# Optimization experiments

Hardware: AMD Instinct MI355X
Metric: run time of the kernel (lower is better)

Reference implementation:

```python
import jax, jax.numpy as jnp
import numpy as np
import math

N_HEADS = 16
FACTOR = 5

def setup_inputs() -> dict:
    key = jax.random.key(0)
    ks = jax.random.split(key, 9)
    B, T, D = 4, 2048, 1024
    w = lambda k: jax.random.normal(k, (D, D), dtype=jnp.float32) * 0.02
    return {
        "x": jax.random.normal(ks[0], (B, T, D), dtype=jnp.float32),
        "Wq": w(ks[1]), "bq": jnp.zeros((D,), jnp.float32),
        "Wk": w(ks[2]), "bk": jnp.zeros((D,), jnp.float32),
        "Wv": w(ks[3]), "bv": jnp.zeros((D,), jnp.float32),
        "Wo": w(ks[4]), "bo": jnp.zeros((D,), jnp.float32),
    }

def reference(x, Wq, bq, Wk, bk, Wv, bv, Wo, bo):
    B, T, D = x.shape
    H = N_HEADS
    hd = D // H
    scale = hd ** (-0.5)

    def proj(W, b):
        # [B,T,D] -> [B,H,T,hd]
        return (x @ W + b).reshape(B, T, H, hd).transpose(0, 2, 1, 3)

    q = proj(Wq, bq)
    k = proj(Wk, bk)
    v = proj(Wv, bv)

    # top-u query selection by L1 norm per (b,h)
    u = min(int(FACTOR * math.log(T)), T)
    q_norm = jnp.sum(jnp.abs(q), axis=-1)          # [B,H,T]
    _, idx = jax.lax.top_k(q_norm, u)              # [B,H,u]

    # gather selected queries; compute only the u selected score rows
    q_sel = jnp.take_along_axis(q, idx[..., None], axis=2)  # [B,H,u,hd]
    sel_scores = jnp.einsum('bhud,bhtd->bhut', q_sel, k) * scale  # [B,H,u,T]

    # causal mask for selected rows: key pos j attends iff j <= query pos
    causal = jnp.arange(T)[None, None, None, :] <= idx[..., None]  # [B,H,u,T]
    sel_scores = jnp.where(causal, sel_scores, -jnp.inf)

    attn = jax.nn.softmax(sel_scores, axis=-1)     # dropout omitted (eval)
    sel_out = jnp.einsum('bhut,bhtd->bhud', attn, v)  # [B,H,u,hd]

    # scatter selected rows back into zeros (non-selected rows stay 0)
    bi = jnp.arange(B)[:, None, None]
    hi = jnp.arange(H)[None, :, None]
    attn_out = jnp.zeros((B, H, T, hd), x.dtype).at[bi, hi, idx].set(sel_out)

    out = attn_out.transpose(0, 2, 1, 3).reshape(B, T, D)
    return out @ Wo + bo
```

## Files before the change

kernel.cpp:

```cpp
#include <hip/hip_runtime.h>
#include <hip/hip_bf16.h>
#include <math.h>

#define B_  4
#define T_  2048
#define D_  1024
#define H_  16
#define HD_ 64
#define U_  38
#define M_  (B_*T_)
#define NCW_ 32
#define NC_ 144

typedef __attribute__((ext_vector_type(8))) short bf16x8;
typedef __attribute__((ext_vector_type(4))) float f32x4;

__device__ __forceinline__ short f2b(float f) {
    __hip_bfloat16 b = __float2bfloat16(f);
    return *(short*)&b;
}
__device__ __forceinline__ float b2f(short s) {
    __hip_bfloat16 b = *(__hip_bfloat16*)&s;
    return __bfloat162float(b);
}
__device__ __forceinline__ unsigned pack2(float lo, float hi) {
    unsigned a = (unsigned short)f2b(lo);
    unsigned b = ((unsigned)(unsigned short)f2b(hi)) << 16;
    return a | b;
}

__device__ __forceinline__ void gload16(const void* g, void* l) {
    __builtin_amdgcn_global_load_lds(
        (const __attribute__((address_space(1))) unsigned int*)g,
        (__attribute__((address_space(3))) unsigned int*)l,
        16, 0, 0);
}

__global__ __launch_bounds__(256) void convx_kernel(
    const float* __restrict__ x, short* __restrict__ xh, short* __restrict__ xl)
{
    const size_t i = ((size_t)blockIdx.x * 256 + threadIdx.x) * 4;
    float4 v = *(const float4*)(x + i);
    short4 h, l;
    h.x = f2b(v.x); l.x = f2b(v.x - b2f(h.x));
    h.y = f2b(v.y); l.y = f2b(v.y - b2f(h.y));
    h.z = f2b(v.z); l.z = f2b(v.z - b2f(h.z));
    h.w = f2b(v.w); l.w = f2b(v.w - b2f(h.w));
    *(short4*)(xh + i) = h;
    *(short4*)(xl + i) = l;
}

__global__ __launch_bounds__(256) void convw_kernel(
    const float* __restrict__ Wq, const float* __restrict__ Wk,
    const float* __restrict__ Wv, const float* __restrict__ Wo,
    short* __restrict__ wq2, short* __restrict__ wkvt, short* __restrict__ wot)
{
    __shared__ float tile[32][33];
    const int which = blockIdx.z;
    const float* W = which == 0 ? Wq : (which == 1 ? Wk : (which == 2 ? Wv : Wo));
    const int k0 = blockIdx.y * 32, n0 = blockIdx.x * 32;
    const int tx = threadIdx.x & 31, ty = threadIdx.x >> 5;
    #pragma unroll
    for (int r = ty; r < 32; r += 8)
        tile[r][tx] = W[(size_t)(k0 + r) * D_ + n0 + tx];
    __syncthreads();
    #pragma unroll
    for (int r = ty; r < 32; r += 8) {
        float v = tile[tx][r];
        size_t o = (size_t)(n0 + r) * D_ + k0 + tx;
        if (which == 0) {
            short h = f2b(v);
            wq2[o] = h;
            wq2[o + 1048576] = f2b(v - b2f(h));
        } else if (which == 3) {
            wot[o] = f2b(v);
        } else {
            wkvt[(size_t)(which - 1) * D_ * D_ + o] = f2b(v);
        }
    }
}

__global__ __launch_bounds__(256) void gemm_fused(
    const short* __restrict__ xh, const short* __restrict__ wq2,
    const short* __restrict__ wkvt,
    const float* __restrict__ bq, const float* __restrict__ bk,
    const float* __restrict__ bv,
    float* __restrict__ qnorm, short* __restrict__ kb, short* __restrict__ vt)
{
    __shared__ short As[128 * 64];
    __shared__ short Bs[128 * 64];
    const int bid = blockIdx.x;
    const bool isQ = bid < 512;
    const int tid = threadIdx.x, wid = tid >> 6, lane = tid & 63;
    const int l15 = lane & 15, gr = lane >> 4;
    const int lb = isQ ? bid : bid - 512;
    const int m0 = (lb & 63) * 128;
    const int n0 = (lb >> 6) * 128;
    const bool isK = !isQ && (n0 < D_);
    const int wr = (wid >> 1) * 64, wc = (wid & 1) * 64;

    f32x4 acc[4][4];
    #pragma unroll
    for (int i = 0; i < 4; ++i)
        #pragma unroll
        for (int j = 0; j < 4; ++j)
            acc[i][j] = (f32x4){0.f, 0.f, 0.f, 0.f};

    const short* Asrc = xh;
    const short* Bsrc = isQ ? wq2 : wkvt;

    for (int kt = 0; kt < 16; ++kt) {
        const int ka = kt * 64;
        #pragma unroll
        for (int i = 0; i < 4; ++i) {
            const int e = tid + i * 256;
            const int row = e >> 3;
            const int soff = ((e & 7) ^ (row & 7)) * 8;
            gload16(Asrc + (size_t)(m0 + row) * D_ + ka + soff,
                    (char*)As + i * 4096 + wid * 1024);
            gload16(Bsrc + (size_t)(n0 + row) * D_ + ka + soff,
                    (char*)Bs + i * 4096 + wid * 1024);
        }
        __syncthreads();
        #pragma unroll
        for (int ks = 0; ks < 2; ++ks) {
            bf16x8 a[4], b[4];
            #pragma unroll
            for (int i = 0; i < 4; ++i)
                a[i] = *(bf16x8*)((char*)As + (wr + i * 16 + l15) * 128
                                   + (((ks << 2) | gr) ^ (l15 & 7)) * 16);
            #pragma unroll
            for (int j = 0; j < 4; ++j)
                b[j] = *(bf16x8*)((char*)Bs + (wc + j * 16 + l15) * 128
                                   + (((ks << 2) | gr) ^ (l15 & 7)) * 16);
            if (isK) {
                #pragma unroll
                for (int i = 0; i < 4; ++i)
                    #pragma unroll
                    for (int j = 0; j < 4; ++j)
                        acc[i][j] = __builtin_amdgcn_mfma_f32_16x16x32_bf16(b[j], a[i], acc[i][j], 0, 0, 0);
            } else {
                #pragma unroll
                for (int i = 0; i < 4; ++i)
                    #pragma unroll
                    for (int j = 0; j < 4; ++j)
                        acc[i][j] = __builtin_amdgcn_mfma_f32_16x16x32_bf16(a[i], b[j], acc[i][j], 0, 0, 0);
            }
        }
        __syncthreads();
    }

    if (isQ) {
        const int h = (n0 + wc) >> 6;
        #pragma unroll
        for (int i = 0; i < 4; ++i)
            #pragma unroll
            for (int r = 0; r < 4; ++r) {
                int row = m0 + wr + i * 16 + gr * 4 + r;
                float s = 0.f;
                #pragma unroll
                for (int j = 0; j < 4; ++j) {
                    int col = n0 + wc + j * 16 + l15;
                    s += fabsf(acc[i][j][r] + bq[col]);
                }
                s += __shfl_xor(s, 1);
                s += __shfl_xor(s, 2);
                s += __shfl_xor(s, 4);
                s += __shfl_xor(s, 8);
                if (l15 == 0) {
                    int b = row >> 11, t = row & (T_ - 1);
                    qnorm[((size_t)b * H_ + h) * T_ + t] = s;
                }
            }
    } else if (isK) {
        #pragma unroll
        for (int i = 0; i < 4; ++i)
            #pragma unroll
            for (int j = 0; j < 4; ++j) {
                const int m = m0 + wr + i * 16 + l15;
                const int bb = m >> 11, t = m & (T_ - 1);
                const int n = n0 + wc + j * 16 + gr * 4;
                const int hh = n >> 6, dd = n & 63;
                float4 bias = *(const float4*)(bk + n);
                short4 pk;
                pk.x = f2b(acc[i][j][0] + bias.x);
                pk.y = f2b(acc[i][j][1] + bias.y);
                pk.z = f2b(acc[i][j][2] + bias.z);
                pk.w = f2b(acc[i][j][3] + bias.w);
                *(short4*)(kb + (((size_t)bb * H_ + hh) * T_ + t) * HD_ + dd) = pk;
            }
    } else {
        #pragma unroll
        for (int i = 0; i < 4; ++i)
            #pragma unroll
            for (int j = 0; j < 4; ++j) {
                const int col = n0 + wc + j * 16 + l15;
                const int rowb = m0 + wr + i * 16 + gr * 4;
                const int bb = rowb >> 11, t0 = rowb & (T_ - 1);
                const int cc2 = col - D_;
                const int hh = cc2 >> 6, dd = cc2 & 63;
                const float bias = bv[cc2];
                short4 pk;
                pk.x = f2b(acc[i][j][0] + bias);
                pk.y = f2b(acc[i][j][1] + bias);
                pk.z = f2b(acc[i][j][2] + bias);
                pk.w = f2b(acc[i][j][3] + bias);
                *(short4*)(vt + (((size_t)bb * H_ + hh) * HD_ + dd) * T_ + t0) = pk;
            }
    }
}

__global__ __launch_bounds__(64) void cand_kernel(
    const float* __restrict__ qnorm, int* __restrict__ cand)
{
    const int g = blockIdx.x;
    const int lane = threadIdx.x;
    unsigned v[32];
    const float* src = qnorm + (size_t)g * T_ + lane * 32;
    #pragma unroll
    for (int i = 0; i < 32; i += 4) {
        float4 t = *(const float4*)(src + i);
        v[i] = __float_as_uint(t.x); v[i + 1] = __float_as_uint(t.y);
        v[i + 2] = __float_as_uint(t.z); v[i + 3] = __float_as_uint(t.w);
    }
    unsigned lo = 0, hi = 0x7F800000u;
    while (lo < hi) {
        unsigned mid = lo + ((hi - lo) >> 1);
        int c = 0;
        #pragma unroll
        for (int i = 0; i < 32; ++i) c += (v[i] >= mid) ? 1 : 0;
        #pragma unroll
        for (int off = 1; off < 64; off <<= 1) c += __shfl_xor(c, off);
        if (c <= NC_) hi = mid; else lo = mid + 1;
    }
    const unsigned tau = lo;
    int myc = 0;
    #pragma unroll
    for (int i = 0; i < 32; ++i) myc += (v[i] >= tau) ? 1 : 0;
    int inc = myc;
    for (int off = 1; off < 64; off <<= 1) {
        int n = __shfl_up(inc, off);
        if (lane >= off) inc += n;
    }
    const int total = __shfl(inc, 63);
    int pos = inc - myc;
    #pragma unroll
    for (int i = 0; i < 32; ++i)
        if (v[i] >= tau) cand[g * NC_ + pos++] = lane * 32 + i;
    for (int p = total + lane; p < NC_; p += 64)
        cand[g * NC_ + p] = -1;
}

__global__ __launch_bounds__(64) void recheck_kernel(
    const short* __restrict__ xh, const short* __restrict__ xl,
    const short* __restrict__ wq2, const float* __restrict__ bq,
    const int* __restrict__ cand,
    float* __restrict__ cnorm, short* __restrict__ candq)
{
    const int blk = blockIdx.x;
    const int g = blk / 9, rt = blk % 9;
    const int b = g >> 4, h = g & 15;
    const int lane = threadIdx.x, l15 = lane & 15, gr = lane >> 4;

    const int aslot = rt * 16 + l15;
    int at = cand[g * NC_ + aslot];
    const size_t arow = ((size_t)b * T_ + (at < 0 ? 0 : at)) * D_;

    f32x4 acc[4];
    #pragma unroll
    for (int j = 0; j < 4; ++j) acc[j] = (f32x4){0.f, 0.f, 0.f, 0.f};

    const short* wqh = wq2;
    const short* wql = wq2 + 1048576;
    for (int kt = 0; kt < 32; ++kt) {
        const int k0 = kt * 32 + gr * 8;
        bf16x8 ah = *(const bf16x8*)(xh + arow + k0);
        bf16x8 al = *(const bf16x8*)(xl + arow + k0);
        #pragma unroll
        for (int j = 0; j < 4; ++j) {
            const size_t wrow = (size_t)(h * HD_ + j * 16 + l15) * D_ + k0;
            bf16x8 bh = *(const bf16x8*)(wqh + wrow);
            bf16x8 bl = *(const bf16x8*)(wql + wrow);
            acc[j] = __builtin_amdgcn_mfma_f32_16x16x32_bf16(ah, bh, acc[j], 0, 0, 0);
            acc[j] = __builtin_amdgcn_mfma_f32_16x16x32_bf16(ah, bl, acc[j], 0, 0, 0);
            acc[j] = __builtin_amdgcn_mfma_f32_16x16x32_bf16(al, bh, acc[j], 0, 0, 0);
        }
    }

    #pragma unroll
    for (int r = 0; r < 4; ++r) {
        const int slot = rt * 16 + gr * 4 + r;
        float s = 0.f;
        #pragma unroll
        for (int j = 0; j < 4; ++j) {
            const int col = j * 16 + l15;
            float val = acc[j][r] + bq[h * HD_ + col];
            candq[((size_t)g * NC_ + slot) * HD_ + col] = f2b(val);
            s += fabsf(val);
        }
        s += __shfl_xor(s, 1);
        s += __shfl_xor(s, 2);
        s += __shfl_xor(s, 4);
        s += __shfl_xor(s, 8);
        if (l15 == 0) {
            int ct = cand[g * NC_ + slot];
            cnorm[g * NC_ + slot] = (ct < 0) ? -3e38f : s;
        }
    }
}

__global__ __launch_bounds__(64) void topk38_kernel(
    const float* __restrict__ cnorm, const int* __restrict__ cand,
    int* __restrict__ idxb, int* __restrict__ slotb)
{
    const int g = blockIdx.x;
    const int lane = threadIdx.x;
    float v[3]; int tt[3];
    #pragma unroll
    for (int i = 0; i < 3; ++i) {
        int s = lane + 64 * i;
        if (s < NC_) {
            v[i] = cnorm[g * NC_ + s];
            int c = cand[g * NC_ + s];
            tt[i] = (c < 0) ? (1 << 30) : c;
            if (c < 0) v[i] = -3e38f;
        } else { v[i] = -3e38f; tt[i] = 1 << 30; }
    }
    for (int it = 0; it < U_; ++it) {
        float bv = -3e38f; int bt = 1 << 30, bi = 0;
        #pragma unroll
        for (int i = 0; i < 3; ++i) {
            bool better = (v[i] > bv) || (v[i] == bv && tt[i] < bt);
            if (better) { bv = v[i]; bt = tt[i]; bi = i; }
        }
        int bs = lane + 64 * bi;
        for (int off = 32; off; off >>= 1) {
            float ov = __shfl_xor(bv, off);
            int ot = __shfl_xor(bt, off);
            int os = __shfl_xor(bs, off);
            if (ov > bv || (ov == bv && ot < bt)) { bv = ov; bt = ot; bs = os; }
        }
        if (lane == 0) { idxb[g * U_ + it] = bt; slotb[g * 40 + it] = bs; }
        if ((bs & 63) == lane) {
            int wi = bs >> 6;
            if (wi == 0) v[0] = -3e38f;
            else if (wi == 1) v[1] = -3e38f;
            else v[2] = -3e38f;
        }
    }
}

__global__ __launch_bounds__(256) void attn_part(
    const short* __restrict__ candq, const int* __restrict__ slotb,
    const short* __restrict__ kb, const short* __restrict__ vt,
    const int* __restrict__ idxb,
    float* __restrict__ pm, float* __restrict__ pl, float* __restrict__ po)
{
    __shared__ short qs[48 * 72];
    __shared__ short pls[4][48 * 72];
    __shared__ int   sidx[48];
    const int bid = blockIdx.x;
    const int g = bid & 63;
    const int c = bid >> 6;
    const int tid = threadIdx.x, wid = tid >> 6, lane = tid & 63;
    const int l15 = lane & 15, gr = lane >> 4;
    const int cw = c * 4 + wid;
    const int j0w = cw * 64;

    if (tid < 48) sidx[tid] = (tid < U_) ? idxb[g * U_ + tid] : 0;
    __syncthreads();
    for (int e = tid; e < 48 * 16; e += 256) {
        int u = e >> 4, d4 = e & 15;
        short4 v = make_short4(0, 0, 0, 0);
        if (u < U_) {
            int slot = slotb[g * 40 + u];
            v = *(const short4*)(candq + ((size_t)g * NC_ + slot) * HD_ + d4 * 4);
        }
        *(short4*)&qs[u * 72 + d4 * 4] = v;
    }
    __syncthreads();

    int su[3];
    #pragma unroll
    for (int uf = 0; uf < 3; ++uf) su[uf] = sidx[uf * 16 + l15];

    f32x4 accs[3][4];
    #pragma unroll
    for (int uf = 0; uf < 3; ++uf)
        #pragma unroll
        for (int jf = 0; jf < 4; ++jf)
            accs[uf][jf] = (f32x4){0.f, 0.f, 0.f, 0.f};

    bf16x8 ka[4][2], qb[3][2];
    #pragma unroll
    for (int jf = 0; jf < 4; ++jf)
        #pragma unroll
        for (int ks = 0; ks < 2; ++ks)
            ka[jf][ks] = *(const bf16x8*)(kb + ((size_t)g * T_ + j0w + jf * 16 + l15) * HD_ + ks * 32 + gr * 8);
    #pragma unroll
    for (int uf = 0; uf < 3; ++uf)
        #pragma unroll
        for (int ks = 0; ks < 2; ++ks)
            qb[uf][ks] = *(bf16x8*)&qs[(uf * 16 + l15) * 72 + ks * 32 + gr * 8];

    #pragma unroll
    for (int uf = 0; uf < 3; ++uf)
        #pragma unroll
        for (int jf = 0; jf < 4; ++jf) {
            accs[uf][jf] = __builtin_amdgcn_mfma_f32_16x16x32_bf16(ka[jf][0], qb[uf][0], accs[uf][jf], 0, 0, 0);
            accs[uf][jf] = __builtin_amdgcn_mfma_f32_16x16x32_bf16(ka[jf][1], qb[uf][1], accs[uf][jf], 0, 0, 0);
        }

    #pragma unroll
    for (int uf = 0; uf < 3; ++uf) {
        float mm = -3e38f;
        #pragma unroll
        for (int jf = 0; jf < 4; ++jf)
            #pragma unroll
            for (int r = 0; r < 4; ++r) {
                int j = j0w + jf * 16 + gr * 4 + r;
                float s = accs[uf][jf][r] * 0.125f;
                s = (j <= su[uf]) ? s : -1e30f;
                accs[uf][jf][r] = s;
                mm = fmaxf(mm, s);
            }
        mm = fmaxf(mm, __shfl_xor(mm, 16));
        mm = fmaxf(mm, __shfl_xor(mm, 32));
        float ll = 0.f;
        #pragma unroll
        for (int jf = 0; jf < 4; ++jf)
            #pragma unroll
            for (int r = 0; r < 4; ++r) {
                float e = __expf(accs[uf][jf][r] - mm);
                accs[uf][jf][r] = e;
                ll += e;
            }
        ll += __shfl_xor(ll, 16);
        ll += __shfl_xor(ll, 32);
        if (gr == 0) {
            int u = uf * 16 + l15;
            if (u < U_) {
                pm[((size_t)g * NCW_ + cw) * U_ + u] = mm;
                pl[((size_t)g * NCW_ + cw) * U_ + u] = ll;
            }
        }
    }

    short* pw = &pls[wid][0];
    #pragma unroll
    for (int uf = 0; uf < 3; ++uf)
        #pragma unroll
        for (int jf = 0; jf < 4; ++jf) {
            uint2 wv;
            wv.x = pack2(accs[uf][jf][0], accs[uf][jf][1]);
            wv.y = pack2(accs[uf][jf][2], accs[uf][jf][3]);
            *(uint2*)&pw[(uf * 16 + l15) * 72 + jf * 16 + gr * 4] = wv;
        }

    bf16x8 va[4][2], pb[3][2];
    #pragma unroll
    for (int df = 0; df < 4; ++df)
        #pragma unroll
        for (int ks = 0; ks < 2; ++ks)
            va[df][ks] = *(const bf16x8*)(vt + ((size_t)g * HD_ + df * 16 + l15) * T_ + j0w + ks * 32 + gr * 8);
    #pragma unroll
    for (int uf = 0; uf < 3; ++uf)
        #pragma unroll
        for (int ks = 0; ks < 2; ++ks)
            pb[uf][ks] = *(bf16x8*)&pw[(uf * 16 + l15) * 72 + ks * 32 + gr * 8];

    f32x4 acco[4][3];
    #pragma unroll
    for (int df = 0; df < 4; ++df)
        #pragma unroll
        for (int uf = 0; uf < 3; ++uf)
            acco[df][uf] = (f32x4){0.f, 0.f, 0.f, 0.f};
    #pragma unroll
    for (int df = 0; df < 4; ++df)
        #pragma unroll
        for (int uf = 0; uf < 3; ++uf) {
            acco[df][uf] = __builtin_amdgcn_mfma_f32_16x16x32_bf16(va[df][0], pb[uf][0], acco[df][uf], 0, 0, 0);
            acco[df][uf] = __builtin_amdgcn_mfma_f32_16x16x32_bf16(va[df][1], pb[uf][1], acco[df][uf], 0, 0, 0);
        }

    #pragma unroll
    for (int df = 0; df < 4; ++df)
        #pragma unroll
        for (int uf = 0; uf < 3; ++uf) {
            int u = uf * 16 + l15;
            if (u < U_) {
                float4 o;
                o.x = acco[df][uf][0]; o.y = acco[df][uf][1];
                o.z = acco[df][uf][2]; o.w = acco[df][uf][3];
                *(float4*)(po + (((size_t)g * NCW_ + cw) * U_ + u) * HD_ + df * 16 + gr * 4) = o;
            }
        }
}

__global__ __launch_bounds__(256) void attn_combine(
    const float* __restrict__ pm, const float* __restrict__ pl,
    const float* __restrict__ po, float* __restrict__ selo)
{
    const int g = blockIdx.x;
    const int u = blockIdx.y * 4 + (threadIdx.x >> 6);
    const int d = threadIdx.x & 63;
    if (u >= U_) return;

    const float* pmg = pm + (size_t)g * NCW_ * U_ + u;
    const float* plg = pl + (size_t)g * NCW_ * U_ + u;

    float mc[NCW_];
    #pragma unroll
    for (int c = 0; c < NCW_; ++c) mc[c] = pmg[(size_t)c * U_];
    float m = -3e38f;
    #pragma unroll
    for (int c = 0; c < NCW_; ++c) m = fmaxf(m, mc[c]);

    float w[NCW_];
    #pragma unroll
    for (int c = 0; c < NCW_; ++c) w[c] = __expf(mc[c] - m);

    float l = 0.f;
    #pragma unroll
    for (int c = 0; c < NCW_; ++c) l += plg[(size_t)c * U_] * w[c];

    float o = 0.f;
    #pragma unroll
    for (int c = 0; c < NCW_; ++c)
        o += po[(((size_t)g * NCW_ + c) * U_ + u) * HD_ + d] * w[c];

    selo[((size_t)g * U_ + u) * HD_ + d] = o / l;
}

__global__ __launch_bounds__(256) void fill_kernel(
    const float* __restrict__ bo, float* __restrict__ out)
{
    const size_t i = (size_t)blockIdx.x * 256 + threadIdx.x;
    float4 bv = *(const float4*)(bo + ((i & 255) << 2));
    *(float4*)(out + i * 4) = bv;
}

__global__ __launch_bounds__(256) void oproj_kernel(
    const float* __restrict__ selo, const int* __restrict__ idxb,
    const short* __restrict__ wot, float* __restrict__ out)
{
    __shared__ short sel[48 * 72];
    __shared__ int st[48];
    const int g = blockIdx.x;
    const int b = g >> 4, h = g & 15;
    const int tid = threadIdx.x, w = tid >> 6, lane = tid & 63;
    const int l15 = lane & 15, gr = lane >> 4;

    for (int e = tid; e < 48 * 16; e += 256) {
        int u = e >> 4, d4 = e & 15;
        short4 v4 = make_short4(0, 0, 0, 0);
        if (u < U_) {
            float4 f = *(const float4*)(selo + ((size_t)g * U_ + u) * HD_ + d4 * 4);
            v4.x = f2b(f.x); v4.y = f2b(f.y); v4.z = f2b(f.z); v4.w = f2b(f.w);
        }
        *(short4*)&sel[u * 72 + d4 * 4] = v4;
    }
    if (tid < 48) st[tid] = (tid < U_) ? idxb[g * U_ + tid] : 0;
    __syncthreads();

    bf16x8 a[3][2];
    #pragma unroll
    for (int uf = 0; uf < 3; ++uf)
        #pragma unroll
        for (int ks = 0; ks < 2; ++ks)
            a[uf][ks] = *(bf16x8*)&sel[(uf * 16 + l15) * 72 + ks * 32 + gr * 8];

    for (int nf = 0; nf < 16; ++nf) {
        const int n0 = w * 256 + nf * 16;
        bf16x8 bf[2];
        #pragma unroll
        for (int ks = 0; ks < 2; ++ks)
            bf[ks] = *(const bf16x8*)(wot + (size_t)(n0 + l15) * D_ + h * HD_ + ks * 32 + gr * 8);
        f32x4 acc[3];
        #pragma unroll
        for (int uf = 0; uf < 3; ++uf) {
            acc[uf] = (f32x4){0.f, 0.f, 0.f, 0.f};
            acc[uf] = __builtin_amdgcn_mfma_f32_16x16x32_bf16(a[uf][0], bf[0], acc[uf], 0, 0, 0);
            acc[uf] = __builtin_amdgcn_mfma_f32_16x16x32_bf16(a[uf][1], bf[1], acc[uf], 0, 0, 0);
        }
        #pragma unroll
        for (int uf = 0; uf < 3; ++uf)
            #pragma unroll
            for (int r = 0; r < 4; ++r) {
                int u = uf * 16 + gr * 4 + r;
                if (u < U_)
                    atomicAdd(out + ((size_t)b * T_ + st[u]) * D_ + n0 + l15, acc[uf][r]);
            }
    }
}

extern "C" void kernel_launch(void* const* d_in, const int* in_sizes, int n_in,
                              void* d_out, int out_size, void* d_ws, size_t ws_size,
                              hipStream_t stream)
{
    const float* x  = (const float*)d_in[0];
    const float* Wq = (const float*)d_in[1];
    const float* bq = (const float*)d_in[2];
    const float* Wk = (const float*)d_in[3];
    const float* bk = (const float*)d_in[4];
    const float* Wv = (const float*)d_in[5];
    const float* bv = (const float*)d_in[6];
    const float* Wo = (const float*)d_in[7];
    const float* bo = (const float*)d_in[8];
    float* out = (float*)d_out;

    char* ws = (char*)d_ws;
    short* xh    = (short*)(ws);
    short* xl    = (short*)(ws + 16777216);
    short* wq2   = (short*)(ws + 33554432);
    short* wkvt  = (short*)(ws + 37748736);
    short* kb    = (short*)(ws + 41943040);
    short* vt    = (short*)(ws + 58720256);
    float* qnorm = (float*)(ws + 75497472);
    int*   idxb  = (int*)  (ws + 76021760);
    float* selo  = (float*)(ws + 76038144);
    int*   cand  = (int*)  (ws + 76660736);
    float* cnorm = (float*)(ws + 76697600);
    int*   slotb = (int*)  (ws + 76734464);
    short* candq = (short*)(ws + 76750848);
    short* wot   = (short*)(ws + 77930496);
    float* po    = (float*)(ws);
    float* pm    = (float*)(ws + 19922944);
    float* pl    = (float*)(ws + 20234240);

    convx_kernel<<<M_ * D_ / 1024, 256, 0, stream>>>(x, xh, xl);
    convw_kernel<<<dim3(32, 32, 4), 256, 0, stream>>>(Wq, Wk, Wv, Wo, wq2, wkvt, wot);
    gemm_fused<<<1536, 256, 0, stream>>>(xh, wq2, wkvt, bq, bk, bv, qnorm, kb, vt);
    cand_kernel<<<B_ * H_, 64, 0, stream>>>(qnorm, cand);
    recheck_kernel<<<B_ * H_ * 9, 64, 0, stream>>>(xh, xl, wq2, bq, cand, cnorm, candq);
    topk38_kernel<<<B_ * H_, 64, 0, stream>>>(cnorm, cand, idxb, slotb);
    attn_part<<<64 * 8, 256, 0, stream>>>(candq, slotb, kb, vt, idxb, pm, pl, po);
    attn_combine<<<dim3(B_ * H_, (U_ + 3) / 4), 256, 0, stream>>>(pm, pl, po, selo);
    fill_kernel<<<(M_ * D_ / 4) / 256, 256, 0, stream>>>(bo, out);
    oproj_kernel<<<B_ * H_, 256, 0, stream>>>(selo, idxb, wot, out);
}
```

Before: 202.7 us.

## Fuse conversion kernels, merge top-k selection stages, reduce attention partials in-block

Merges the x and weight conversion kernels into one launch. Folds candidate selection, the candidate recheck GEMM and the top-38 pick into a single 256-thread block per (batch, head), with intermediates kept in shared memory. Inside attn_part, the four waves' softmax partials are combined in shared memory so only 8 partials per head, not 32, go to global memory for attn_combine. This cuts launch overhead and partial traffic, but the select stage now runs on only 64 blocks, with the 9 recheck tiles spread over 4 waves, which lowers parallelism.

```diff
diff --git a/kernel.cpp b/kernel.cpp
--- a/kernel.cpp
+++ b/kernel.cpp
@@ -9,7 +9,7 @@
 #define HD_ 64
 #define U_  38
 #define M_  (B_*T_)
-#define NCW_ 32
+#define NCB_ 8
 #define NC_ 144
 
 typedef __attribute__((ext_vector_type(8))) short bf16x8;
@@ -36,29 +36,32 @@
         16, 0, 0);
 }
 
-__global__ __launch_bounds__(256) void convx_kernel(
-    const float* __restrict__ x, short* __restrict__ xh, short* __restrict__ xl)
-{
-    const size_t i = ((size_t)blockIdx.x * 256 + threadIdx.x) * 4;
-    float4 v = *(const float4*)(x + i);
-    short4 h, l;
-    h.x = f2b(v.x); l.x = f2b(v.x - b2f(h.x));
-    h.y = f2b(v.y); l.y = f2b(v.y - b2f(h.y));
-    h.z = f2b(v.z); l.z = f2b(v.z - b2f(h.z));
-    h.w = f2b(v.w); l.w = f2b(v.w - b2f(h.w));
-    *(short4*)(xh + i) = h;
-    *(short4*)(xl + i) = l;
-}
-
-__global__ __launch_bounds__(256) void convw_kernel(
+__global__ __launch_bounds__(256) void conv_fused(
+    const float* __restrict__ x,
     const float* __restrict__ Wq, const float* __restrict__ Wk,
     const float* __restrict__ Wv, const float* __restrict__ Wo,
+    short* __restrict__ xh, short* __restrict__ xl,
     short* __restrict__ wq2, short* __restrict__ wkvt, short* __restrict__ wot)
 {
     __shared__ float tile[32][33];
-    const int which = blockIdx.z;
+    const int bid = blockIdx.x;
+    if (bid < 8192) {
+        const size_t i = ((size_t)bid * 256 + threadIdx.x) * 4;
+        float4 v = *(const float4*)(x + i);
+        short4 h, l;
+        h.x = f2b(v.x); l.x = f2b(v.x - b2f(h.x));
+        h.y = f2b(v.y); l.y = f2b(v.y - b2f(h.y));
+        h.z = f2b(v.z); l.z = f2b(v.z - b2f(h.z));
+        h.w = f2b(v.w); l.w = f2b(v.w - b2f(h.w));
+        *(short4*)(xh + i) = h;
+        *(short4*)(xl + i) = l;
+        return;
+    }
+    const int q = bid - 8192;
+    const int which = q >> 10;
+    const int by = (q & 1023) >> 5, bx = q & 31;
     const float* W = which == 0 ? Wq : (which == 1 ? Wk : (which == 2 ? Wv : Wo));
-    const int k0 = blockIdx.y * 32, n0 = blockIdx.x * 32;
+    const int k0 = by * 32, n0 = bx * 32;
     const int tx = threadIdx.x & 31, ty = threadIdx.x >> 5;
     #pragma unroll
     for (int r = ty; r < 32; r += 8)
@@ -210,142 +213,133 @@
     }
 }
 
-__global__ __launch_bounds__(64) void cand_kernel(
-    const float* __restrict__ qnorm, int* __restrict__ cand)
-{
-    const int g = blockIdx.x;
-    const int lane = threadIdx.x;
-    unsigned v[32];
-    const float* src = qnorm + (size_t)g * T_ + lane * 32;
-    #pragma unroll
-    for (int i = 0; i < 32; i += 4) {
-        float4 t = *(const float4*)(src + i);
-        v[i] = __float_as_uint(t.x); v[i + 1] = __float_as_uint(t.y);
-        v[i + 2] = __float_as_uint(t.z); v[i + 3] = __float_as_uint(t.w);
-    }
-    unsigned lo = 0, hi = 0x7F800000u;
-    while (lo < hi) {
-        unsigned mid = lo + ((hi - lo) >> 1);
-        int c = 0;
-        #pragma unroll
-        for (int i = 0; i < 32; ++i) c += (v[i] >= mid) ? 1 : 0;
-        #pragma unroll
-        for (int off = 1; off < 64; off <<= 1) c += __shfl_xor(c, off);
-        if (c <= NC_) hi = mid; else lo = mid + 1;
-    }
-    const unsigned tau = lo;
-    int myc = 0;
-    #pragma unroll
-    for (int i = 0; i < 32; ++i) myc += (v[i] >= tau) ? 1 : 0;
-    int inc = myc;
-    for (int off = 1; off < 64; off <<= 1) {
-        int n = __shfl_up(inc, off);
-        if (lane >= off) inc += n;
-    }
-    const int total = __shfl(inc, 63);
-    int pos = inc - myc;
-    #pragma unroll
-    for (int i = 0; i < 32; ++i)
-        if (v[i] >= tau) cand[g * NC_ + pos++] = lane * 32 + i;
-    for (int p = total + lane; p < NC_; p += 64)
-        cand[g * NC_ + p] = -1;
-}
-
-__global__ __launch_bounds__(64) void recheck_kernel(
+__global__ __launch_bounds__(256) void select_kernel(
+    const float* __restrict__ qnorm,
     const short* __restrict__ xh, const short* __restrict__ xl,
     const short* __restrict__ wq2, const float* __restrict__ bq,
-    const int* __restrict__ cand,
-    float* __restrict__ cnorm, short* __restrict__ candq)
-{
-    const int blk = blockIdx.x;
-    const int g = blk / 9, rt = blk % 9;
+    int* __restrict__ idxb, int* __restrict__ slotb, short* __restrict__ candq)
+{
+    __shared__ int   scand[NC_];
+    __shared__ float scnorm[NC_];
+    const int g = blockIdx.x;
     const int b = g >> 4, h = g & 15;
-    const int lane = threadIdx.x, l15 = lane & 15, gr = lane >> 4;
-
-    const int aslot = rt * 16 + l15;
-    int at = cand[g * NC_ + aslot];
-    const size_t arow = ((size_t)b * T_ + (at < 0 ? 0 : at)) * D_;
-
-    f32x4 acc[4];
-    #pragma unroll
-    for (int j = 0; j < 4; ++j) acc[j] = (f32x4){0.f, 0.f, 0.f, 0.f};
+    const int tid = threadIdx.x, wid = tid >> 6, lane = tid & 63;
+    const int l15 = lane & 15, gr = lane >> 4;
+
+    if (wid == 0) {
+        unsigned v[32];
+        const float* src = qnorm + (size_t)g * T_ + lane * 32;
+        #pragma unroll
+        for (int i = 0; i < 32; i += 4) {
+            float4 t = *(const float4*)(src + i);
+            v[i] = __float_as_uint(t.x); v[i + 1] = __float_as_uint(t.y);
+            v[i + 2] = __float_as_uint(t.z); v[i + 3] = __float_as_uint(t.w);
+        }
+        unsigned lo = 0, hi = 0x7F800000u;
+        while (lo < hi) {
+            unsigned mid = lo + ((hi - lo) >> 1);
+            int c = 0;
+            #pragma unroll
+            for (int i = 0; i < 32; ++i) c += (v[i] >= mid) ? 1 : 0;
+            #pragma unroll
+            for (int off = 1; off < 64; off <<= 1) c += __shfl_xor(c, off);
+            if (c <= NC_) hi = mid; else lo = mid + 1;
+        }
+        const unsigned tau = lo;
+        int myc = 0;
+        #pragma unroll
+        for (int i = 0; i < 32; ++i) myc += (v[i] >= tau) ? 1 : 0;
+        int inc = myc;
+        for (int off = 1; off < 64; off <<= 1) {
+            int n = __shfl_up(inc, off);
+            if (lane >= off) inc += n;
+        }
+        const int total = __shfl(inc, 63);
+        int pos = inc - myc;
+        #pragma unroll
+        for (int i = 0; i < 32; ++i)
+            if (v[i] >= tau) scand[pos++] = lane * 32 + i;
+        for (int p = total + lane; p < NC_; p += 64)
+            scand[p] = -1;
+    }
+    __syncthreads();
 
     const short* wqh = wq2;
     const short* wql = wq2 + 1048576;
-    for (int kt = 0; kt < 32; ++kt) {
-        const int k0 = kt * 32 + gr * 8;
-        bf16x8 ah = *(const bf16x8*)(xh + arow + k0);
-        bf16x8 al = *(const bf16x8*)(xl + arow + k0);
-        #pragma unroll
-        for (int j = 0; j < 4; ++j) {
-            const size_t wrow = (size_t)(h * HD_ + j * 16 + l15) * D_ + k0;
-            bf16x8 bh = *(const bf16x8*)(wqh + wrow);
-            bf16x8 bl = *(const bf16x8*)(wql + wrow);
-            acc[j] = __builtin_amdgcn_mfma_f32_16x16x32_bf16(ah, bh, acc[j], 0, 0, 0);
-            acc[j] = __builtin_amdgcn_mfma_f32_16x16x32_bf16(ah, bl, acc[j], 0, 0, 0);
-            acc[j] = __builtin_amdgcn_mfma_f32_16x16x32_bf16(al, bh, acc[j], 0, 0, 0);
-        }
-    }
-
-    #pragma unroll
-    for (int r = 0; r < 4; ++r) {
-        const int slot = rt * 16 + gr * 4 + r;
-        float s = 0.f;
-        #pragma unroll
-        for (int j = 0; j < 4; ++j) {
-            const int col = j * 16 + l15;
-            float val = acc[j][r] + bq[h * HD_ + col];
-            candq[((size_t)g * NC_ + slot) * HD_ + col] = f2b(val);
-            s += fabsf(val);
-        }
-        s += __shfl_xor(s, 1);
-        s += __shfl_xor(s, 2);
-        s += __shfl_xor(s, 4);
-        s += __shfl_xor(s, 8);
-        if (l15 == 0) {
-            int ct = cand[g * NC_ + slot];
-            cnorm[g * NC_ + slot] = (ct < 0) ? -3e38f : s;
-        }
-    }
-}
-
-__global__ __launch_bounds__(64) void topk38_kernel(
-    const float* __restrict__ cnorm, const int* __restrict__ cand,
-    int* __restrict__ idxb, int* __restrict__ slotb)
-{
-    const int g = blockIdx.x;
-    const int lane = threadIdx.x;
-    float v[3]; int tt[3];
-    #pragma unroll
-    for (int i = 0; i < 3; ++i) {
-        int s = lane + 64 * i;
-        if (s < NC_) {
-            v[i] = cnorm[g * NC_ + s];
-            int c = cand[g * NC_ + s];
-            tt[i] = (c < 0) ? (1 << 30) : c;
-            if (c < 0) v[i] = -3e38f;
-        } else { v[i] = -3e38f; tt[i] = 1 << 30; }
-    }
-    for (int it = 0; it < U_; ++it) {
-        float bv = -3e38f; int bt = 1 << 30, bi = 0;
+    for (int rt = wid; rt < 9; rt += 4) {
+        int at = scand[rt * 16 + l15];
+        const size_t arow = ((size_t)b * T_ + (at < 0 ? 0 : at)) * D_;
+        f32x4 acc[4];
+        #pragma unroll
+        for (int j = 0; j < 4; ++j) acc[j] = (f32x4){0.f, 0.f, 0.f, 0.f};
+        for (int kt = 0; kt < 32; ++kt) {
+            const int k0 = kt * 32 + gr * 8;
+            bf16x8 ah = *(const bf16x8*)(xh + arow + k0);
+            bf16x8 al = *(const bf16x8*)(xl + arow + k0);
+            #pragma unroll
+            for (int j = 0; j < 4; ++j) {
+                const size_t wrow = (size_t)(h * HD_ + j * 16 + l15) * D_ + k0;
+                bf16x8 bh = *(const bf16x8*)(wqh + wrow);
+                bf16x8 bl = *(const bf16x8*)(wql + wrow);
+                acc[j] = __builtin_amdgcn_mfma_f32_16x16x32_bf16(ah, bh, acc[j], 0, 0, 0);
+                acc[j] = __builtin_amdgcn_mfma_f32_16x16x32_bf16(ah, bl, acc[j], 0, 0, 0);
+                acc[j] = __builtin_amdgcn_mfma_f32_16x16x32_bf16(al, bh, acc[j], 0, 0, 0);
+            }
+        }
+        #pragma unroll
+        for (int r = 0; r < 4; ++r) {
+            const int slot = rt * 16 + gr * 4 + r;
+            float s = 0.f;
+            #pragma unroll
+            for (int j = 0; j < 4; ++j) {
+                const int col = j * 16 + l15;
+                float val = acc[j][r] + bq[h * HD_ + col];
+                candq[((size_t)g * NC_ + slot) * HD_ + col] = f2b(val);
+                s += fabsf(val);
+            }
+            s += __shfl_xor(s, 1);
+            s += __shfl_xor(s, 2);
+            s += __shfl_xor(s, 4);
+            s += __shfl_xor(s, 8);
+            if (l15 == 0)
+                scnorm[slot] = (scand[slot] < 0) ? -3e38f : s;
+        }
+    }
+    __syncthreads();
+
+    if (wid == 0) {
+        float v[3]; int tt[3];
         #pragma unroll
         for (int i = 0; i < 3; ++i) {
-            bool better = (v[i] > bv) || (v[i] == bv && tt[i] < bt);
-            if (better) { bv = v[i]; bt = tt[i]; bi = i; }
-        }
-        int bs = lane + 64 * bi;
-        for (int off = 32; off; off >>= 1) {
-            float ov = __shfl_xor(bv, off);
-            int ot = __shfl_xor(bt, off);
-            int os = __shfl_xor(bs, off);
-            if (ov > bv || (ov == bv && ot < bt)) { bv = ov; bt = ot; bs = os; }
-        }
-        if (lane == 0) { idxb[g * U_ + it] = bt; slotb[g * 40 + it] = bs; }
-        if ((bs & 63) == lane) {
-            int wi = bs >> 6;
-            if (wi == 0) v[0] = -3e38f;
-            else if (wi == 1) v[1] = -3e38f;
-            else v[2] = -3e38f;
+            int s = lane + 64 * i;
+            if (s < NC_) {
+                v[i] = scnorm[s];
+                int c = scand[s];
+                tt[i] = (c < 0) ? (1 << 30) : c;
+                if (c < 0) v[i] = -3e38f;
+            } else { v[i] = -3e38f; tt[i] = 1 << 30; }
+        }
+        for (int it = 0; it < U_; ++it) {
+            float bv = -3e38f; int bt = 1 << 30, bi = 0;
+            #pragma unroll
+            for (int i = 0; i < 3; ++i) {
+                bool better = (v[i] > bv) || (v[i] == bv && tt[i] < bt);
+                if (better) { bv = v[i]; bt = tt[i]; bi = i; }
+            }
+            int bs = lane + 64 * bi;
+            for (int off = 32; off; off >>= 1) {
+                float ov = __shfl_xor(bv, off);
+                int ot = __shfl_xor(bt, off);
+                int os = __shfl_xor(bs, off);
+                if (ov > bv || (ov == bv && ot < bt)) { bv = ov; bt = ot; bs = os; }
+            }
+            if (lane == 0) { idxb[g * U_ + it] = bt; slotb[g * 40 + it] = bs; }
+            if ((bs & 63) == lane) {
+                int wi = bs >> 6;
+                if (wi == 0) v[0] = -3e38f;
+                else if (wi == 1) v[1] = -3e38f;
+                else v[2] = -3e38f;
+            }
         }
     }
 }
@@ -357,15 +351,19 @@
     float* __restrict__ pm, float* __restrict__ pl, float* __restrict__ po)
 {
     __shared__ short qs[48 * 72];
-    __shared__ short pls[4][48 * 72];
-    __shared__ int   sidx[48];
+    __shared__ __align__(16) char shbuf[40448];
+    __shared__ int sidx[48];
+    short* pls  = (short*)shbuf;
+    float* redo = (float*)shbuf;
+    float* redm = (float*)(shbuf + 38912);
+    float* redl = (float*)(shbuf + 39680);
+
     const int bid = blockIdx.x;
     const int g = bid & 63;
     const int c = bid >> 6;
     const int tid = threadIdx.x, wid = tid >> 6, lane = tid & 63;
     const int l15 = lane & 15, gr = lane >> 4;
-    const int cw = c * 4 + wid;
-    const int j0w = cw * 64;
+    const int j0w = (c * 4 + wid) * 64;
 
     if (tid < 48) sidx[tid] = (tid < U_) ? idxb[g * U_ + tid] : 0;
     __syncthreads();
@@ -439,14 +437,12 @@
         ll += __shfl_xor(ll, 32);
         if (gr == 0) {
             int u = uf * 16 + l15;
-            if (u < U_) {
-                pm[((size_t)g * NCW_ + cw) * U_ + u] = mm;
-                pl[((size_t)g * NCW_ + cw) * U_ + u] = ll;
-            }
-        }
-    }
-
-    short* pw = &pls[wid][0];
+            redm[wid * 48 + u] = mm;
+            redl[wid * 48 + u] = ll;
+        }
+    }
+
+    short* pw = pls + wid * 48 * 72;
     #pragma unroll
     for (int uf = 0; uf < 3; ++uf)
         #pragma unroll
@@ -482,6 +478,8 @@
             acco[df][uf] = __builtin_amdgcn_mfma_f32_16x16x32_bf16(va[df][0], pb[uf][0], acco[df][uf], 0, 0, 0);
             acco[df][uf] = __builtin_amdgcn_mfma_f32_16x16x32_bf16(va[df][1], pb[uf][1], acco[df][uf], 0, 0, 0);
         }
+
+    __syncthreads();
 
     #pragma unroll
     for (int df = 0; df < 4; ++df)
@@ -492,9 +490,27 @@
                 float4 o;
                 o.x = acco[df][uf][0]; o.y = acco[df][uf][1];
                 o.z = acco[df][uf][2]; o.w = acco[df][uf][3];
-                *(float4*)(po + (((size_t)g * NCW_ + cw) * U_ + u) * HD_ + df * 16 + gr * 4) = o;
-            }
-        }
+                *(float4*)&redo[((size_t)(wid * 38 + u)) * 64 + df * 16 + gr * 4] = o;
+            }
+        }
+    __syncthreads();
+
+    for (int e = tid; e < U_ * 64; e += 256) {
+        int u = e >> 6, d = e & 63;
+        float m0 = redm[u], m1 = redm[48 + u], m2 = redm[96 + u], m3 = redm[144 + u];
+        float m = fmaxf(fmaxf(m0, m1), fmaxf(m2, m3));
+        float e0 = __expf(m0 - m), e1 = __expf(m1 - m), e2 = __expf(m2 - m), e3 = __expf(m3 - m);
+        float l = redl[u] * e0 + redl[48 + u] * e1 + redl[96 + u] * e2 + redl[144 + u] * e3;
+        float o = redo[(size_t)u * 64 + d] * e0
+                + redo[(size_t)(38 + u) * 64 + d] * e1
+                + redo[(size_t)(76 + u) * 64 + d] * e2
+                + redo[(size_t)(114 + u) * 64 + d] * e3;
+        po[((size_t)(g * NCB_ + c) * U_ + u) * HD_ + d] = o;
+        if (d == 0) {
+            pm[(size_t)(g * NCB_ + c) * U_ + u] = m;
+            pl[(size_t)(g * NCB_ + c) * U_ + u] = l;
+        }
+    }
 }
 
 __global__ __launch_bounds__(256) void attn_combine(
@@ -506,28 +522,28 @@
     const int d = threadIdx.x & 63;
     if (u >= U_) return;
 
-    const float* pmg = pm + (size_t)g * NCW_ * U_ + u;
-    const float* plg = pl + (size_t)g * NCW_ * U_ + u;
-
-    float mc[NCW_];
-    #pragma unroll
-    for (int c = 0; c < NCW_; ++c) mc[c] = pmg[(size_t)c * U_];
+    const float* pmg = pm + (size_t)g * NCB_ * U_ + u;
+    const float* plg = pl + (size_t)g * NCB_ * U_ + u;
+
+    float mc[NCB_];
+    #pragma unroll
+    for (int c = 0; c < NCB_; ++c) mc[c] = pmg[(size_t)c * U_];
     float m = -3e38f;
     #pragma unroll
-    for (int c = 0; c < NCW_; ++c) m = fmaxf(m, mc[c]);
-
-    float w[NCW_];
-    #pragma unroll
-    for (int c = 0; c < NCW_; ++c) w[c] = __expf(mc[c] - m);
+    for (int c = 0; c < NCB_; ++c) m = fmaxf(m, mc[c]);
+
+    float w[NCB_];
+    #pragma unroll
+    for (int c = 0; c < NCB_; ++c) w[c] = __expf(mc[c] - m);
 
     float l = 0.f;
     #pragma unroll
-    for (int c = 0; c < NCW_; ++c) l += plg[(size_t)c * U_] * w[c];
+    for (int c = 0; c < NCB_; ++c) l += plg[(size_t)c * U_] * w[c];
 
     float o = 0.f;
     #pragma unroll
-    for (int c = 0; c < NCW_; ++c)
-        o += po[(((size_t)g * NCW_ + c) * U_ + u) * HD_ + d] * w[c];
+    for (int c = 0; c < NCB_; ++c)
+        o += po[(((size_t)g * NCB_ + c) * U_ + u) * HD_ + d] * w[c];
 
     selo[((size_t)g * U_ + u) * HD_ + d] = o / l;
 }
@@ -619,8 +635,6 @@
     float* qnorm = (float*)(ws + 75497472);
     int*   idxb  = (int*)  (ws + 76021760);
     float* selo  = (float*)(ws + 76038144);
-    int*   cand  = (int*)  (ws + 76660736);
-    float* cnorm = (float*)(ws + 76697600);
     int*   slotb = (int*)  (ws + 76734464);
     short* candq = (short*)(ws + 76750848);
     short* wot   = (short*)(ws + 77930496);
@@ -628,13 +642,12 @@
     float* pm    = (float*)(ws + 19922944);
     float* pl    = (float*)(ws + 20234240);
 
-    convx_kernel<<<M_ * D_ / 1024, 256, 0, stream>>>(x, xh, xl);
-    convw_kernel<<<dim3(32, 32, 4), 256, 0, stream>>>(Wq, Wk, Wv, Wo, wq2, wkvt, wot);
+    conv_fused<<<8192 + 4096, 256, 0, stream>>>(x, Wq, Wk, Wv, Wo,
+                                                xh, xl, wq2, wkvt, wot);
     gemm_fused<<<1536, 256, 0, stream>>>(xh, wq2, wkvt, bq, bk, bv, qnorm, kb, vt);
-    cand_kernel<<<B_ * H_, 64, 0, stream>>>(qnorm, cand);
-    recheck_kernel<<<B_ * H_ * 9, 64, 0, stream>>>(xh, xl, wq2, bq, cand, cnorm, candq);
-    topk38_kernel<<<B_ * H_, 64, 0, stream>>>(cnorm, cand, idxb, slotb);
-    attn_part<<<64 * 8, 256, 0, stream>>>(candq, slotb, kb, vt, idxb, pm, pl, po);
+    select_kernel<<<B_ * H_, 256, 0, stream>>>(qnorm, xh, xl, wq2, bq,
+                                               idxb, slotb, candq);
+    attn_part<<<64 * NCB_, 256, 0, stream>>>(candq, slotb, kb, vt, idxb, pm, pl, po);
     attn_combine<<<dim3(B_ * H_, (U_ + 3) / 4), 256, 0, stream>>>(pm, pl, po, selo);
     fill_kernel<<<(M_ * D_ / 4) / 256, 256, 0, stream>>>(bo, out);
     oproj_kernel<<<B_ * H_, 256, 0, stream>>>(selo, idxb, wot, out);
```

Result: slower. 306.5 us (+51.2%).
